# Optimization experiments

Hardware: AMD Instinct MI355X
Metric: run time of the kernel (lower is better)

Reference implementation:

```python
import jax, jax.numpy as jnp
import numpy as np

N_NODES = 50000
N_EDGES = 800000
F_IN = 64
HID = 128
N_GRAPHS = 64
F_OUT = 1
NEG_SLOPE = 0.2


def _glorot(key, shape):
    fan_in, fan_out = shape[0], shape[-1]
    s = jnp.sqrt(6.0 / (fan_in + fan_out))
    return jax.random.uniform(key, shape, jnp.float32, -s, s)


def setup_inputs() -> dict:
    key = jax.random.key(0)
    ks = jax.random.split(key, 24)
    inp = {
        "x": jax.random.normal(ks[0], (N_NODES, F_IN), jnp.float32),
        "edge_index": jax.random.randint(ks[1], (2, N_EDGES), 0, N_NODES, jnp.int32),
        "edge_weight": jax.random.uniform(ks[2], (N_EDGES, 1), jnp.float32),
        "batch": jnp.sort(jax.random.randint(ks[3], (N_NODES,), 0, N_GRAPHS, jnp.int32)),
        # GATv2Conv layer 1 (heads=1): lin_l, lin_r (with bias), lin_edge (no bias), att, out-bias
        "W1l": _glorot(ks[4], (F_IN, HID)), "b1l": jnp.zeros((HID,), jnp.float32),
        "W1r": _glorot(ks[5], (F_IN, HID)), "b1r": jnp.zeros((HID,), jnp.float32),
        "We1": _glorot(ks[6], (1, HID)),
        "att1": _glorot(ks[7], (HID, 1))[:, 0],
        "bias1": jnp.zeros((HID,), jnp.float32),
        # GATv2Conv layer 2
        "W2l": _glorot(ks[8], (HID, HID)), "b2l": jnp.zeros((HID,), jnp.float32),
        "W2r": _glorot(ks[9], (HID, HID)), "b2r": jnp.zeros((HID,), jnp.float32),
        "We2": _glorot(ks[10], (1, HID)),
        "att2": _glorot(ks[11], (HID, 1))[:, 0],
        "bias2": jnp.zeros((HID,), jnp.float32),
        # final Linear
        "Wlin": _glorot(ks[12], (HID, F_OUT)),
        "blin": jnp.zeros((F_OUT,), jnp.float32),
    }
    return inp


def gatv2_layer(x, src, dst, eattr, Wl, bl, Wr, br, We, att, bias):
    n = x.shape[0]
    # add_self_loops=True with edge_attr fill_value='mean'
    loop = jnp.arange(n, dtype=src.dtype)
    src = jnp.concatenate([src, loop])
    dst = jnp.concatenate([dst, loop])
    mean_attr = jnp.mean(eattr, axis=0, keepdims=True)  # [1, edge_dim]
    eattr = jnp.concatenate([eattr, jnp.broadcast_to(mean_attr, (n, eattr.shape[1]))])
    xl = x @ Wl + bl            # [N, HID] source transform
    xr = x @ Wr + br            # [N, HID] dest transform
    ee = eattr @ We             # [E', HID] edge embedding
    m = jax.nn.leaky_relu(xl[src] + xr[dst] + ee, NEG_SLOPE)  # [E', HID]
    logits = m @ att            # [E']
    # per-destination softmax (every node has a self loop, so no empty segments)
    lmax = jax.ops.segment_max(logits, dst, num_segments=n)
    w = jnp.exp(logits - lmax[dst])
    denom = jax.ops.segment_sum(w, dst, num_segments=n)
    alpha = w / denom[dst]
    out = jax.ops.segment_sum(xl[src] * alpha[:, None], dst, num_segments=n)
    return out + bias


def reference(x, edge_index, edge_weight, batch,
              W1l, b1l, W1r, b1r, We1, att1, bias1,
              W2l, b2l, W2r, b2r, We2, att2, bias2,
              Wlin, blin):
    src, dst = edge_index[0], edge_index[1]
    h = jax.nn.relu(gatv2_layer(x, src, dst, edge_weight, W1l, b1l, W1r, b1r, We1, att1, bias1))
    h = jax.nn.relu(gatv2_layer(h, src, dst, edge_weight, W2l, b2l, W2r, b2r, We2, att2, bias2))
    # global_mean_pool over graph assignment
    sums = jax.ops.segment_sum(h, batch, num_segments=N_GRAPHS)
    cnt = jax.ops.segment_sum(jnp.ones((h.shape[0],), h.dtype), batch, num_segments=N_GRAPHS)
    pooled = sums / jnp.maximum(cnt, 1.0)[:, None]
    return pooled @ Wlin + blin  # [N_GRAPHS, F_OUT]
```

## Files before the change

kernel.cpp:

```cpp
#include <hip/hip_runtime.h>

#define NN 50000
#define NE 800000
#define EP (NE + NN)
#define HID 128
#define FIN 64
#define NG 64
#define SLOPE 0.2f
#define NB 49

typedef unsigned short ushort_t;
typedef unsigned int uint_t;
typedef __attribute__((ext_vector_type(8))) short bf16x8;
typedef __attribute__((ext_vector_type(4))) float f32x4;

__device__ __forceinline__ float wred_sum(float v) {
  for (int off = 32; off; off >>= 1) v += __shfl_xor(v, off);
  return v;
}
__device__ __forceinline__ ushort_t f2bf(float f) {
  uint_t b = __float_as_uint(f);
  b += 0x7fffu + ((b >> 16) & 1u);
  return (ushort_t)(b >> 16);
}
__device__ __forceinline__ float bf2f(ushort_t u) {
  return __uint_as_float((uint_t)u << 16);
}

__global__ void k_cvt(const float* __restrict__ x, ushort_t* __restrict__ x16) {
  int i = blockIdx.x * blockDim.x + threadIdx.x;
  float4 v = *(const float4*)(x + (size_t)i * 4);
  ushort4 u;
  u.x = f2bf(v.x); u.y = f2bf(v.y); u.z = f2bf(v.z); u.w = f2bf(v.w);
  *(ushort4*)(x16 + (size_t)i * 4) = u;
}

__global__ void k_packW(const float* __restrict__ W, ushort_t* __restrict__ WP,
                        int K) {
  int i = blockIdx.x * blockDim.x + threadIdx.x;
  if (i >= K * HID) return;
  int k = i / HID, nn = i % HID;
  WP[((size_t)(k >> 5) * HID + nn) * 32 + (k & 31)] = f2bf(W[i]);
}

__global__ void k_hist2(const int* __restrict__ edst, const float* __restrict__ ew,
                        int* __restrict__ counts, float* __restrict__ meansum) {
  int tid = blockIdx.x * blockDim.x + threadIdx.x;
  int stride = gridDim.x * blockDim.x;
  float s = 0.f;
  for (int i = tid; i < NE; i += stride) {
    atomicAdd(&counts[edst[i]], 1);
    s += ew[i];
  }
  s = wred_sum(s);
  if ((threadIdx.x & 63) == 0) atomicAdd(meansum, s);
}

__global__ __launch_bounds__(1024) void k_scan1(const int* __restrict__ counts,
                                                int* __restrict__ starts,
                                                int* __restrict__ bsum) {
  __shared__ int wsum[16];
  __shared__ int woff[16];
  int t = threadIdx.x, lane = t & 63, w = t >> 6;
  int i = blockIdx.x * 1024 + t;
  int v = (i < NN) ? counts[i] + 1 : 0;
  int sc = v;
  #pragma unroll
  for (int d = 1; d < 64; d <<= 1) {
    int u = __shfl_up(sc, d);
    if (lane >= d) sc += u;
  }
  if (lane == 63) wsum[w] = sc;
  __syncthreads();
  if (w == 0 && lane < 16) {
    int x = wsum[lane];
    #pragma unroll
    for (int d = 1; d < 16; d <<= 1) {
      int u = __shfl_up(x, d);
      if (lane >= d) x += u;
    }
    woff[lane] = x;
  }
  __syncthreads();
  int waveoff = (w == 0) ? 0 : woff[w - 1];
  if (i < NN) starts[i] = waveoff + sc - v;
  if (t == 1023) bsum[blockIdx.x] = woff[15];
}

__global__ void k_scan2(int* __restrict__ bsum, int* __restrict__ starts) {
  int t = threadIdx.x;
  int v = (t < NB) ? bsum[t] : 0;
  int sc = v;
  #pragma unroll
  for (int d = 1; d < 64; d <<= 1) {
    int u = __shfl_up(sc, d);
    if (t >= d) sc += u;
  }
  if (t < NB) bsum[t] = sc - v;
  if (t == 0) starts[NN] = EP;
}

__global__ __launch_bounds__(1024) void k_scan3(int* __restrict__ starts,
                                                const int* __restrict__ bsum,
                                                int* __restrict__ counts) {
  int i = blockIdx.x * 1024 + threadIdx.x;
  if (i < NN) {
    starts[i] += bsum[blockIdx.x];
    counts[i] = 0;
  }
}

__global__ void k_scatter(const int* __restrict__ esrc, const int* __restrict__ edst,
                          const float* __restrict__ ew, const float* __restrict__ meansum,
                          const int* __restrict__ starts, int* __restrict__ cursor,
                          int2* __restrict__ emeta) {
  float mw = meansum[0] * (1.0f / NE);
  int tid = blockIdx.x * blockDim.x + threadIdx.x;
  int stride = gridDim.x * blockDim.x;
  for (int i = tid; i < EP; i += stride) {
    int s, d; float wv;
    if (i < NE) { s = esrc[i]; d = edst[i]; wv = ew[i]; }
    else        { s = d = i - NE; wv = mw; }
    int pos = starts[d] + atomicAdd(&cursor[d], 1);
    emeta[pos] = make_int2(s, __float_as_int(wv));
  }
}

template <int K>
__global__ __launch_bounds__(256) void k_gemmM(const ushort_t* __restrict__ A16,
                                               const ushort_t* __restrict__ WPl,
                                               const float* __restrict__ bl,
                                               const ushort_t* __restrict__ WPr,
                                               const float* __restrict__ br,
                                               ushort_t* __restrict__ xlout,
                                               float* __restrict__ xrout, int n) {
  int t = threadIdx.x;
  int wave = t >> 6, lane = t & 63;
  int m = lane & 15, kb = lane >> 4;
  int row0 = blockIdx.x * 64 + wave * 16;
  int ra = min(row0 + m, n - 1);
  f32x4 acc[16];
  #pragma unroll
  for (int i = 0; i < 16; ++i) acc[i] = (f32x4)(0.f);
  #pragma unroll
  for (int kt = 0; kt < K / 32; ++kt) {
    bf16x8 a = *(const bf16x8*)(A16 + (size_t)ra * K + kt * 32 + kb * 8);
    #pragma unroll
    for (int nf = 0; nf < 8; ++nf) {
      bf16x8 bfr = *(const bf16x8*)(WPl + ((size_t)kt * HID + nf * 16 + m) * 32 + kb * 8);
      acc[nf] = __builtin_amdgcn_mfma_f32_16x16x32_bf16(a, bfr, acc[nf], 0, 0, 0);
    }
    #pragma unroll
    for (int nf = 0; nf < 8; ++nf) {
      bf16x8 bfr = *(const bf16x8*)(WPr + ((size_t)kt * HID + nf * 16 + m) * 32 + kb * 8);
      acc[8 + nf] = __builtin_amdgcn_mfma_f32_16x16x32_bf16(a, bfr, acc[8 + nf], 0, 0, 0);
    }
  }
  #pragma unroll
  for (int nf = 0; nf < 8; ++nf) {
    int col = nf * 16 + m;
    float bbl = bl[col], bbr = br[col];
    #pragma unroll
    for (int j = 0; j < 4; ++j) {
      int r = row0 + kb * 4 + j;
      if (r < n) {
        xlout[(size_t)r * HID + col] = f2bf(acc[nf][j] + bbl);
        xrout[(size_t)r * HID + col] = acc[8 + nf][j] + bbr;
      }
    }
  }
}

__global__ __launch_bounds__(256, 4) void k_fused(const ushort_t* __restrict__ xl16,
                                                  const float* __restrict__ xr,
                                                  const int2* __restrict__ emeta,
                                                  const int* __restrict__ starts,
                                                  const float* __restrict__ We,
                                                  const float* __restrict__ att,
                                                  const float* __restrict__ bias,
                                                  ushort_t* __restrict__ hout) {
  int node = blockIdx.x * (blockDim.x >> 6) + (threadIdx.x >> 6);
  int lane = threadIdx.x & 63;
  if (node >= NN) return;
  int hl = lane & 31;
  int half = lane >> 5;
  int s0 = starts[node], s1 = starts[node + 1];
  int f = hl * 4;
  float4 xro = *(const float4*)(xr + (size_t)node * HID + f);
  float4 we  = *(const float4*)(We + f);
  float4 at  = *(const float4*)(att + f);

  int emy = 8 * half + ((hl >> 2) & 7);
  bool b4 = (hl & 16) != 0;
  bool b3 = (hl & 8) != 0;
  bool b2 = (hl & 4) != 0;

  float ssum = 0.f;
  float4 acc = make_float4(0.f, 0.f, 0.f, 0.f);

  for (int i0 = s0; i0 < s1; i0 += 16) {
    int base = i0 + 8 * half;
    uint2 g[8];
    float p[8];
    #pragma unroll
    for (int k = 0; k < 8; ++k) {
      int idx = min(base + k, s1 - 1);
      int2 em = emeta[idx];
      p[k] = __int_as_float(em.y);
      g[k] = *(const uint2*)(xl16 + (size_t)em.x * HID + f);
    }
    #pragma unroll
    for (int k = 0; k < 8; ++k) {
      float wk = p[k];
      float t0 = __uint_as_float(g[k].x << 16)          + xro.x + wk * we.x;
      float t1 = __uint_as_float(g[k].x & 0xffff0000u)  + xro.y + wk * we.y;
      float t2 = __uint_as_float(g[k].y << 16)          + xro.z + wk * we.z;
      float t3 = __uint_as_float(g[k].y & 0xffff0000u)  + xro.w + wk * we.w;
      t0 = t0 > 0.f ? t0 : SLOPE * t0;
      t1 = t1 > 0.f ? t1 : SLOPE * t1;
      t2 = t2 > 0.f ? t2 : SLOPE * t2;
      t3 = t3 > 0.f ? t3 : SLOPE * t3;
      p[k] = t0 * at.x + t1 * at.y + t2 * at.z + t3 * at.w;
    }
    float sdv, rcv;
    float q0, q1, q2, q3;
    sdv = b4 ? p[0] : p[4]; rcv = __shfl_xor(sdv, 16, 32); q0 = (b4 ? p[4] : p[0]) + rcv;
    sdv = b4 ? p[1] : p[5]; rcv = __shfl_xor(sdv, 16, 32); q1 = (b4 ? p[5] : p[1]) + rcv;
    sdv = b4 ? p[2] : p[6]; rcv = __shfl_xor(sdv, 16, 32); q2 = (b4 ? p[6] : p[2]) + rcv;
    sdv = b4 ? p[3] : p[7]; rcv = __shfl_xor(sdv, 16, 32); q3 = (b4 ? p[7] : p[3]) + rcv;
    float r0, r1;
    sdv = b3 ? q0 : q2; rcv = __shfl_xor(sdv, 8, 32); r0 = (b3 ? q2 : q0) + rcv;
    sdv = b3 ? q1 : q3; rcv = __shfl_xor(sdv, 8, 32); r1 = (b3 ? q3 : q1) + rcv;
    sdv = b2 ? r0 : r1; rcv = __shfl_xor(sdv, 4, 32);
    float lg = (b2 ? r1 : r0) + rcv;
    lg += __shfl_xor(lg, 1, 32);
    lg += __shfl_xor(lg, 2, 32);
    float w = (i0 + emy < s1) ? __expf(lg) : 0.f;
    ssum += w;
    #pragma unroll
    for (int k = 0; k < 8; ++k) {
      float wk = __shfl(w, k << 2, 32);
      acc.x += wk * __uint_as_float(g[k].x << 16);
      acc.y += wk * __uint_as_float(g[k].x & 0xffff0000u);
      acc.z += wk * __uint_as_float(g[k].y << 16);
      acc.w += wk * __uint_as_float(g[k].y & 0xffff0000u);
    }
  }
  acc.x += __shfl_xor(acc.x, 32);
  acc.y += __shfl_xor(acc.y, 32);
  acc.z += __shfl_xor(acc.z, 32);
  acc.w += __shfl_xor(acc.w, 32);
  float st = wred_sum(ssum) * 0.25f;
  float inv = 1.0f / st;
  if (half == 0) {
    float4 bb = *(const float4*)(bias + f);
    ushort4 u;
    u.x = f2bf(fmaxf(acc.x * inv + bb.x, 0.f));
    u.y = f2bf(fmaxf(acc.y * inv + bb.y, 0.f));
    u.z = f2bf(fmaxf(acc.z * inv + bb.z, 0.f));
    u.w = f2bf(fmaxf(acc.w * inv + bb.w, 0.f));
    *(ushort4*)(hout + (size_t)node * HID + f) = u;
  }
}

__global__ void k_bounds(const int* __restrict__ batch, int* __restrict__ gs) {
  int i = blockIdx.x * blockDim.x + threadIdx.x;
  if (i >= NN) return;
  int b = batch[i];
  if (i == 0) {
    for (int g = 0; g <= b; ++g) gs[g] = 0;
  }
  int bn = (i + 1 < NN) ? batch[i + 1] : NG;
  for (int g = b + 1; g <= bn; ++g) gs[g] = i + 1;
}

__global__ __launch_bounds__(256) void k_pool(const ushort_t* __restrict__ h,
                                              const int* __restrict__ gs,
                                              const float* __restrict__ Wlin,
                                              const float* __restrict__ blin,
                                              float* __restrict__ out) {
  __shared__ float red[256];
  int g = blockIdx.x;
  int t = threadIdx.x;
  int f = t & 127;
  int half = t >> 7;
  int n0 = gs[g], n1 = gs[g + 1];
  float s0 = 0.f, s1 = 0.f, s2 = 0.f, s3 = 0.f;
  int n = n0 + half;
  for (; n + 6 < n1; n += 8) {
    s0 += bf2f(h[(size_t)n * HID + f]);
    s1 += bf2f(h[(size_t)(n + 2) * HID + f]);
    s2 += bf2f(h[(size_t)(n + 4) * HID + f]);
    s3 += bf2f(h[(size_t)(n + 6) * HID + f]);
  }
  for (; n < n1; n += 2) s0 += bf2f(h[(size_t)n * HID + f]);
  red[t] = (s0 + s1) + (s2 + s3);
  __syncthreads();
  if (t < 128) {
    float pooled = red[t] + red[t + 128];
    float cnt = (float)max(n1 - n0, 1);
    red[t] = (pooled / cnt) * Wlin[f];
  }
  __syncthreads();
  if (t < 64) {
    float v = red[t] + red[t + 64];
    v = wred_sum(v);
    if (t == 0) out[g] = v + blin[0];
  }
}

extern "C" void kernel_launch(void* const* d_in, const int* in_sizes, int n_in,
                              void* d_out, int out_size, void* d_ws, size_t ws_size,
                              hipStream_t stream) {
  const float* x     = (const float*)d_in[0];
  const int*   ei    = (const int*)d_in[1];
  const float* ew    = (const float*)d_in[2];
  const int*   batch = (const int*)d_in[3];
  const float* W1l = (const float*)d_in[4];
  const float* b1l = (const float*)d_in[5];
  const float* W1r = (const float*)d_in[6];
  const float* b1r = (const float*)d_in[7];
  const float* We1 = (const float*)d_in[8];
  const float* at1 = (const float*)d_in[9];
  const float* bi1 = (const float*)d_in[10];
  const float* W2l = (const float*)d_in[11];
  const float* b2l = (const float*)d_in[12];
  const float* W2r = (const float*)d_in[13];
  const float* b2r = (const float*)d_in[14];
  const float* We2 = (const float*)d_in[15];
  const float* at2 = (const float*)d_in[16];
  const float* bi2 = (const float*)d_in[17];
  const float* Wlin = (const float*)d_in[18];
  const float* blin = (const float*)d_in[19];

  float* ws = (float*)d_ws;
  size_t o = 0;
  float*    xr    = ws + o; o += (size_t)NN * HID;
  ushort_t* xl16  = (ushort_t*)(ws + o); o += (size_t)NN * HID / 2;
  ushort_t* hb16  = (ushort_t*)(ws + o); o += (size_t)NN * HID / 2;
  ushort_t* x16   = (ushort_t*)(ws + o); o += (size_t)NN * FIN / 2;
  ushort_t* WP1l  = (ushort_t*)(ws + o); o += (size_t)FIN * HID / 2;
  ushort_t* WP1r  = (ushort_t*)(ws + o); o += (size_t)FIN * HID / 2;
  ushort_t* WP2l  = (ushort_t*)(ws + o); o += (size_t)HID * HID / 2;
  ushort_t* WP2r  = (ushort_t*)(ws + o); o += (size_t)HID * HID / 2;
  int2*     emeta = (int2*)(ws + o); o += (size_t)2 * EP;
  int*      starts = (int*)(ws + o); o += NN + 1;
  int*      gs     = (int*)(ws + o); o += NG + 1;
  int*      bsum   = (int*)(ws + o); o += NB;
  size_t zoff = o;
  int*      counts  = (int*)(ws + o); o += NN;
  float*    meansum = ws + o; o += 1;
  size_t zero_bytes = (o - zoff) * sizeof(float);

  hipMemsetAsync(counts, 0, zero_bytes, stream);

  k_cvt<<<(NN * FIN / 4) / 256, 256, 0, stream>>>(x, x16);
  k_packW<<<(FIN * HID + 255) / 256, 256, 0, stream>>>(W1l, WP1l, FIN);
  k_packW<<<(FIN * HID + 255) / 256, 256, 0, stream>>>(W1r, WP1r, FIN);
  k_packW<<<(HID * HID + 255) / 256, 256, 0, stream>>>(W2l, WP2l, HID);
  k_packW<<<(HID * HID + 255) / 256, 256, 0, stream>>>(W2r, WP2r, HID);

  k_hist2<<<1024, 256, 0, stream>>>(ei + NE, ew, counts, meansum);
  k_scan1<<<NB, 1024, 0, stream>>>(counts, starts, bsum);
  k_scan2<<<1, 64, 0, stream>>>(bsum, starts);
  k_scan3<<<NB, 1024, 0, stream>>>(starts, bsum, counts);
  k_scatter<<<1024, 256, 0, stream>>>(ei, ei + NE, ew, meansum, starts, counts,
                                      emeta);
  k_bounds<<<(NN + 255) / 256, 256, 0, stream>>>(batch, gs);

  int gb  = (NN + 63) / 64;
  int nbn = (NN + 3) / 4;

  k_gemmM<FIN><<<gb, 256, 0, stream>>>(x16, WP1l, b1l, WP1r, b1r, xl16, xr, NN);
  k_fused<<<nbn, 256, 0, stream>>>(xl16, xr, emeta, starts, We1, at1, bi1, hb16);
  k_gemmM<HID><<<gb, 256, 0, stream>>>(hb16, WP2l, b2l, WP2r, b2r, xl16, xr, NN);
  k_fused<<<nbn, 256, 0, stream>>>(xl16, xr, emeta, starts, We2, at2, bi2, hb16);
  k_pool<<<NG, 256, 0, stream>>>(hb16, gs, Wlin, blin, (float*)d_out);
}
```

Baseline: 394.1 us.

## Double-buffer edge gathers in fused GAT kernel and merge small prep launches

```diff
diff --git a/kernel.cpp b/kernel.cpp
--- a/kernel.cpp
+++ b/kernel.cpp
@@ -27,20 +27,45 @@
   return __uint_as_float((uint_t)u << 16);
 }
 
-__global__ void k_cvt(const float* __restrict__ x, ushort_t* __restrict__ x16) {
+__global__ void k_prep(const float* __restrict__ x, ushort_t* __restrict__ x16,
+                       const float* __restrict__ W1l, ushort_t* __restrict__ WP1l,
+                       const float* __restrict__ W1r, ushort_t* __restrict__ WP1r,
+                       const float* __restrict__ W2l, ushort_t* __restrict__ WP2l,
+                       const float* __restrict__ W2r, ushort_t* __restrict__ WP2r) {
   int i = blockIdx.x * blockDim.x + threadIdx.x;
-  float4 v = *(const float4*)(x + (size_t)i * 4);
-  ushort4 u;
-  u.x = f2bf(v.x); u.y = f2bf(v.y); u.z = f2bf(v.z); u.w = f2bf(v.w);
-  *(ushort4*)(x16 + (size_t)i * 4) = u;
-}
-
-__global__ void k_packW(const float* __restrict__ W, ushort_t* __restrict__ WP,
-                        int K) {
-  int i = blockIdx.x * blockDim.x + threadIdx.x;
-  if (i >= K * HID) return;
-  int k = i / HID, nn = i % HID;
-  WP[((size_t)(k >> 5) * HID + nn) * 32 + (k & 31)] = f2bf(W[i]);
+  const int R0 = NN * FIN / 4;
+  const int RS = FIN * HID;
+  const int RB = HID * HID;
+  if (i < R0) {
+    float4 v = *(const float4*)(x + (size_t)i * 4);
+    ushort4 u;
+    u.x = f2bf(v.x); u.y = f2bf(v.y); u.z = f2bf(v.z); u.w = f2bf(v.w);
+    *(ushort4*)(x16 + (size_t)i * 4) = u;
+    return;
+  }
+  i -= R0;
+  if (i < RS) {
+    int k = i / HID, nn = i % HID;
+    WP1l[((size_t)(k >> 5) * HID + nn) * 32 + (k & 31)] = f2bf(W1l[i]);
+    return;
+  }
+  i -= RS;
+  if (i < RS) {
+    int k = i / HID, nn = i % HID;
+    WP1r[((size_t)(k >> 5) * HID + nn) * 32 + (k & 31)] = f2bf(W1r[i]);
+    return;
+  }
+  i -= RS;
+  if (i < RB) {
+    int k = i / HID, nn = i % HID;
+    WP2l[((size_t)(k >> 5) * HID + nn) * 32 + (k & 31)] = f2bf(W2l[i]);
+    return;
+  }
+  i -= RB;
+  if (i < RB) {
+    int k = i / HID, nn = i % HID;
+    WP2r[((size_t)(k >> 5) * HID + nn) * 32 + (k & 31)] = f2bf(W2r[i]);
+  }
 }
 
 __global__ void k_hist2(const int* __restrict__ edst, const float* __restrict__ ew,
@@ -102,11 +127,19 @@
 
 __global__ __launch_bounds__(1024) void k_scan3(int* __restrict__ starts,
                                                 const int* __restrict__ bsum,
-                                                int* __restrict__ counts) {
+                                                int* __restrict__ counts,
+                                                const int* __restrict__ batch,
+                                                int* __restrict__ gs) {
   int i = blockIdx.x * 1024 + threadIdx.x;
   if (i < NN) {
     starts[i] += bsum[blockIdx.x];
     counts[i] = 0;
+    int b = batch[i];
+    if (i == 0) {
+      for (int g = 0; g <= b; ++g) gs[g] = 0;
+    }
+    int bn = (i + 1 < NN) ? batch[i + 1] : NG;
+    for (int g = b + 1; g <= bn; ++g) gs[g] = i + 1;
   }
 }
 
@@ -171,7 +204,7 @@
   }
 }
 
-__global__ __launch_bounds__(256, 4) void k_fused(const ushort_t* __restrict__ xl16,
+__global__ __launch_bounds__(256, 2) void k_fused(const ushort_t* __restrict__ xl16,
                                                   const float* __restrict__ xr,
                                                   const int2* __restrict__ emeta,
                                                   const int* __restrict__ starts,
@@ -198,10 +231,8 @@
   float ssum = 0.f;
   float4 acc = make_float4(0.f, 0.f, 0.f, 0.f);
 
-  for (int i0 = s0; i0 < s1; i0 += 16) {
+  auto loadset = [&](uint2 (&g)[8], float (&p)[8], int i0) {
     int base = i0 + 8 * half;
-    uint2 g[8];
-    float p[8];
     #pragma unroll
     for (int k = 0; k < 8; ++k) {
       int idx = min(base + k, s1 - 1);
@@ -209,6 +240,8 @@
       p[k] = __int_as_float(em.y);
       g[k] = *(const uint2*)(xl16 + (size_t)em.x * HID + f);
     }
+  };
+  auto process = [&](uint2 (&g)[8], float (&p)[8], int i0) {
     #pragma unroll
     for (int k = 0; k < 8; ++k) {
       float wk = p[k];
@@ -245,7 +278,26 @@
       acc.z += wk * __uint_as_float(g[k].y << 16);
       acc.w += wk * __uint_as_float(g[k].y & 0xffff0000u);
     }
-  }
+  };
+
+  uint2 gA[8], gB[8];
+  float pA[8], pB[8];
+  int i0 = s0;
+  loadset(gA, pA, i0);
+  while (true) {
+    int i1 = i0 + 16;
+    bool haveB = (i1 < s1);
+    if (haveB) loadset(gB, pB, i1);
+    process(gA, pA, i0);
+    if (!haveB) break;
+    int i2 = i1 + 16;
+    bool haveA = (i2 < s1);
+    if (haveA) loadset(gA, pA, i2);
+    process(gB, pB, i1);
+    if (!haveA) break;
+    i0 = i2;
+  }
+
   acc.x += __shfl_xor(acc.x, 32);
   acc.y += __shfl_xor(acc.y, 32);
   acc.z += __shfl_xor(acc.z, 32);
@@ -261,17 +313,6 @@
     u.w = f2bf(fmaxf(acc.w * inv + bb.w, 0.f));
     *(ushort4*)(hout + (size_t)node * HID + f) = u;
   }
-}
-
-__global__ void k_bounds(const int* __restrict__ batch, int* __restrict__ gs) {
-  int i = blockIdx.x * blockDim.x + threadIdx.x;
-  if (i >= NN) return;
-  int b = batch[i];
-  if (i == 0) {
-    for (int g = 0; g <= b; ++g) gs[g] = 0;
-  }
-  int bn = (i + 1 < NN) ? batch[i + 1] : NG;
-  for (int g = b + 1; g <= bn; ++g) gs[g] = i + 1;
 }
 
 __global__ __launch_bounds__(256) void k_pool(const ushort_t* __restrict__ h,
@@ -354,19 +395,16 @@
 
   hipMemsetAsync(counts, 0, zero_bytes, stream);
 
-  k_cvt<<<(NN * FIN / 4) / 256, 256, 0, stream>>>(x, x16);
-  k_packW<<<(FIN * HID + 255) / 256, 256, 0, stream>>>(W1l, WP1l, FIN);
-  k_packW<<<(FIN * HID + 255) / 256, 256, 0, stream>>>(W1r, WP1r, FIN);
-  k_packW<<<(HID * HID + 255) / 256, 256, 0, stream>>>(W2l, WP2l, HID);
-  k_packW<<<(HID * HID + 255) / 256, 256, 0, stream>>>(W2r, WP2r, HID);
+  const int PREP = NN * FIN / 4 + 2 * FIN * HID + 2 * HID * HID;
+  k_prep<<<(PREP + 255) / 256, 256, 0, stream>>>(x, x16, W1l, WP1l, W1r, WP1r,
+                                                 W2l, WP2l, W2r, WP2r);
 
   k_hist2<<<1024, 256, 0, stream>>>(ei + NE, ew, counts, meansum);
   k_scan1<<<NB, 1024, 0, stream>>>(counts, starts, bsum);
   k_scan2<<<1, 64, 0, stream>>>(bsum, starts);
-  k_scan3<<<NB, 1024, 0, stream>>>(starts, bsum, counts);
+  k_scan3<<<NB, 1024, 0, stream>>>(starts, bsum, counts, batch, gs);
   k_scatter<<<1024, 256, 0, stream>>>(ei, ei + NE, ew, meansum, starts, counts,
                                       emeta);
-  k_bounds<<<(NN + 255) / 256, 256, 0, stream>>>(batch, gs);
 
   int gb  = (NN + 63) / 64;
   int nbn = (NN + 3) / 4;
```

After: 396.9 us. About the same (+0.7%).
